# Kernel optimization log

Hardware: AMD Instinct MI355X
Metric: run time of the kernel (lower is better)

Reference implementation:

```python
import math
import jax, jax.numpy as jnp
import numpy as np

N_LAYERS = 2
D_MODEL = 512
D_STATE = 16
D_CONV = 4
D_INNER = 2 * D_MODEL          # expand = 2
DT_RANK = math.ceil(D_MODEL / 16)
BATCH = 16
SEQ = 2048
NUM_CLASSES = 1


def setup_inputs() -> dict:
    key = jax.random.key(0)
    ks = jax.random.split(key, 9)
    def rn(k, shape, scale=0.02):
        return jax.random.normal(k, shape, dtype=jnp.float32) * scale
    src       = jax.random.normal(ks[0], (BATCH, SEQ, D_MODEL), dtype=jnp.float32)
    norm_w    = jnp.ones((N_LAYERS, D_MODEL), jnp.float32)
    in_proj_W = rn(ks[1], (N_LAYERS, 2 * D_INNER, D_MODEL))
    conv_W    = rn(ks[2], (N_LAYERS, D_INNER, D_CONV), 0.1)
    conv_b    = jnp.zeros((N_LAYERS, D_INNER), jnp.float32)
    x_proj_W  = rn(ks[3], (N_LAYERS, DT_RANK + 2 * D_STATE, D_INNER))
    dt_proj_W = rn(ks[4], (N_LAYERS, D_INNER, DT_RANK), DT_RANK ** -0.5)
    dt_proj_b = rn(ks[5], (N_LAYERS, D_INNER), 0.1)
    # S4D-real init: A_n = n for n = 1..d_state, stored as log
    A_log     = jnp.log(jnp.broadcast_to(
        jnp.arange(1, D_STATE + 1, dtype=jnp.float32), (N_LAYERS, D_INNER, D_STATE)))
    D_skip    = jnp.ones((N_LAYERS, D_INNER), jnp.float32)
    out_proj_W = rn(ks[6], (N_LAYERS, D_MODEL, D_INNER))
    cls_W     = rn(ks[7], (NUM_CLASSES, D_MODEL))
    cls_b     = jnp.zeros((NUM_CLASSES,), jnp.float32)
    return dict(src=src, norm_w=norm_w, in_proj_W=in_proj_W, conv_W=conv_W,
                conv_b=conv_b, x_proj_W=x_proj_W, dt_proj_W=dt_proj_W,
                dt_proj_b=dt_proj_b, A_log=A_log, D_skip=D_skip,
                out_proj_W=out_proj_W, cls_W=cls_W, cls_b=cls_b)


def _rmsnorm(x, w, eps=1e-5):
    return x * jax.lax.rsqrt(jnp.mean(x * x, axis=-1, keepdims=True) + eps) * w


def _mamba_block(x, p):
    B, L, _ = x.shape
    xz = jnp.einsum('bld,ed->ble', x, p['in_proj_W'])      # (B,L,2*ED)
    xb, z = jnp.split(xz, 2, axis=-1)
    # causal depthwise conv along time
    xc = jax.lax.conv_general_dilated(
        xb.transpose(0, 2, 1), p['conv_W'][:, None, :], (1,),
        [(D_CONV - 1, 0)], feature_group_count=D_INNER,
        dimension_numbers=('NCH', 'OIH', 'NCH'))
    xc = (xc + p['conv_b'][None, :, None]).transpose(0, 2, 1)  # (B,L,ED)
    xc = jax.nn.silu(xc)
    # input-dependent SSM params
    dbc = jnp.einsum('ble,re->blr', xc, p['x_proj_W'])
    dt, Bm, Cm = jnp.split(dbc, [DT_RANK, DT_RANK + D_STATE], axis=-1)
    delta = jax.nn.softplus(
        jnp.einsum('blr,er->ble', dt, p['dt_proj_W']) + p['dt_proj_b'])
    A = -jnp.exp(p['A_log'])                                # (ED,N)

    def step(h, inp):
        d_t, B_t, C_t, x_t = inp                            # (B,ED),(B,N),(B,N),(B,ED)
        dA = jnp.exp(d_t[:, :, None] * A)                   # (B,ED,N)
        h = dA * h + d_t[:, :, None] * B_t[:, None, :] * x_t[:, :, None]
        y = jnp.einsum('ben,bn->be', h, C_t)
        return h, y

    h0 = jnp.zeros((B, D_INNER, D_STATE), xc.dtype)
    xs = (delta.transpose(1, 0, 2), Bm.transpose(1, 0, 2),
          Cm.transpose(1, 0, 2), xc.transpose(1, 0, 2))
    _, ys = jax.lax.scan(step, h0, xs)                      # (L,B,ED)
    y = ys.transpose(1, 0, 2) + p['D_skip'] * xc
    y = y * jax.nn.silu(z)
    return jnp.einsum('ble,de->bld', y, p['out_proj_W'])


def reference(src, norm_w, in_proj_W, conv_W, conv_b, x_proj_W, dt_proj_W,
              dt_proj_b, A_log, D_skip, out_proj_W, cls_W, cls_b):
    x = src
    for l in range(N_LAYERS):
        p = dict(in_proj_W=in_proj_W[l], conv_W=conv_W[l], conv_b=conv_b[l],
                 x_proj_W=x_proj_W[l], dt_proj_W=dt_proj_W[l],
                 dt_proj_b=dt_proj_b[l], A_log=A_log[l], D_skip=D_skip[l],
                 out_proj_W=out_proj_W[l])
        x = x + _mamba_block(_rmsnorm(x, norm_w[l]), p)
    pooled = x.mean(axis=1)                                  # (B, d_model)
    logits = pooled @ cls_W.T + cls_b
    return jax.nn.sigmoid(logits)
```

## Files before the change

### kernel.cpp

```cpp
#include <hip/hip_runtime.h>
#include <math.h>

#define DEV __device__ __forceinline__

constexpr int B_ = 16, L_ = 2048, DM = 512, DI = 1024, DS = 16;
constexpr int G_ = 64, CS = L_ / G_;

using f32x4  = __attribute__((ext_vector_type(4))) float;
using f2     = __attribute__((ext_vector_type(2))) float;
using bf16x8 = __attribute__((ext_vector_type(8))) __bf16;

DEV float bf2f(unsigned int u) { return __uint_as_float(u << 16); }
DEV unsigned short f2bf(float f) {
  unsigned u = __float_as_uint(f);
  u += 0x7fff + ((u >> 16) & 1);
  return (unsigned short)(u >> 16);
}
DEV float sigm(float x) { return 1.f / (1.f + __expf(-x)); }

constexpr size_t O_NORM  = 0;
constexpr size_t O_INPJ  = 1024;
constexpr size_t O_CONVW = 2098176;
constexpr size_t O_CONVB = 2106368;
constexpr size_t O_XPJ   = 2108416;
constexpr size_t O_DTW   = 2239488;
constexpr size_t O_DTB   = 2305024;
constexpr size_t O_ALOG  = 2307072;
constexpr size_t O_DSK   = 2339840;
constexpr size_t O_OUTW  = 2341888;
constexpr size_t O_CLSW  = 3390464;
constexpr size_t O_CLSB  = 3390976;
constexpr size_t CW_TOT  = 3390977;

DEV unsigned short cvt1(const void* p, size_t i, int bf) {
  return bf ? ((const unsigned short*)p)[i] : f2bf(((const float*)p)[i]);
}

__global__ void k_cvtw(const void* normw, const void* inpj, const void* convw, const void* convb,
                       const void* xpj,   const void* dtw,  const void* dtb,   const void* alog,
                       const void* dsk,   const void* outw, const void* clsw,  const void* clsb,
                       int* __restrict__ flag, float* __restrict__ logits,
                       unsigned short* __restrict__ dst) {
  const unsigned short* nw = (const unsigned short*)normw;
  int bf = 1;
  #pragma unroll
  for (int i = 0; i < 8; i += 2) bf &= (nw[i] == 0x3F80);
  size_t i = (size_t)blockIdx.x * 256 + threadIdx.x;
  if (i == 0) *flag = bf;
  if (i < 16 * 256) logits[i] = 0.f;
  if (i >= CW_TOT) return;
  unsigned short v;
  if      (i < O_INPJ)  v = cvt1(normw, i - O_NORM,  bf);
  else if (i < O_CONVW) v = cvt1(inpj,  i - O_INPJ,  bf);
  else if (i < O_CONVB) v = cvt1(convw, i - O_CONVW, bf);
  else if (i < O_XPJ)   v = cvt1(convb, i - O_CONVB, bf);
  else if (i < O_DTW)   v = cvt1(xpj,   i - O_XPJ,   bf);
  else if (i < O_DTB)   v = cvt1(dtw,   i - O_DTW,   bf);
  else if (i < O_ALOG)  v = cvt1(dtb,   i - O_DTB,   bf);
  else if (i < O_DSK)   v = cvt1(alog,  i - O_ALOG,  bf);
  else if (i < O_OUTW)  v = cvt1(dsk,   i - O_DSK,   bf);
  else if (i < O_CLSW)  v = cvt1(outw,  i - O_OUTW,  bf);
  else if (i < O_CLSB)  v = cvt1(clsw,  i - O_CLSW,  bf);
  else                  v = cvt1(clsb,  i - O_CLSB,  bf);
  dst[i] = v;
}

__global__ void k_rmsnorm0(const unsigned short* __restrict__ s16, const float* __restrict__ s32,
                           const int* __restrict__ flag, const unsigned short* __restrict__ w,
                           unsigned short* __restrict__ out, float* __restrict__ x) {
  int t = blockIdx.x, tid = threadIdx.x;
  int d = tid * 2;
  float2 v;
  if (*flag) {
    ushort2 u = ((const ushort2*)(s16 + (size_t)t * DM))[tid];
    v.x = bf2f(u.x); v.y = bf2f(u.y);
  } else {
    v = ((const float2*)(s32 + (size_t)t * DM))[tid];
  }
  ((float2*)(x + (size_t)t * DM))[tid] = v;
  float ss = v.x * v.x + v.y * v.y;
  #pragma unroll
  for (int m = 32; m; m >>= 1) ss += __shfl_xor(ss, m, 64);
  __shared__ float sr[4];
  if ((tid & 63) == 0) sr[tid >> 6] = ss;
  __syncthreads();
  float scale = rsqrtf((sr[0] + sr[1] + sr[2] + sr[3]) * (1.f / DM) + 1e-5f);
  unsigned short o0 = f2bf(v.x * scale * bf2f(w[d]));
  unsigned short o1 = f2bf(v.y * scale * bf2f(w[d + 1]));
  *(ushort2*)(out + (size_t)t * DM + d) = make_ushort2(o0, o1);
}

__global__ void k_rmsnorm1(const float* __restrict__ x, const unsigned short* __restrict__ w,
                           const unsigned short* __restrict__ clsW, float* __restrict__ lg,
                           unsigned short* __restrict__ out) {
  int t = blockIdx.x, tid = threadIdx.x;
  float2 v = ((const float2*)(x + (size_t)t * DM))[tid];
  int d = tid * 2;
  float ss = v.x * v.x + v.y * v.y;
  float cd = v.x * bf2f(clsW[d]) + v.y * bf2f(clsW[d + 1]);
  #pragma unroll
  for (int m = 32; m; m >>= 1) {
    ss += __shfl_xor(ss, m, 64);
    cd += __shfl_xor(cd, m, 64);
  }
  __shared__ float sr[4], sc[4];
  if ((tid & 63) == 0) { sr[tid >> 6] = ss; sc[tid >> 6] = cd; }
  __syncthreads();
  float scale = rsqrtf((sr[0] + sr[1] + sr[2] + sr[3]) * (1.f / DM) + 1e-5f);
  if (tid == 0)
    atomicAdd(&lg[(t >> 11) * 256 + (t & 255)], sc[0] + sc[1] + sc[2] + sc[3]);
  unsigned short o0 = f2bf(v.x * scale * bf2f(w[d]));
  unsigned short o1 = f2bf(v.y * scale * bf2f(w[d + 1]));
  *(ushort2*)(out + (size_t)t * DM + d) = make_ushort2(o0, o1);
}

DEV void async16(const void* g, void* l) {
  __builtin_amdgcn_global_load_lds((const __attribute__((address_space(1))) unsigned int*)g,
                                   (__attribute__((address_space(3))) unsigned int*)l, 16, 0, 0);
}

template <int BM, int BN, int EPI>
__global__ __launch_bounds__(256)
void k_gemm(const unsigned short* __restrict__ A, const unsigned short* __restrict__ B,
            void* __restrict__ C, int K, int lda, int ldb, int ldc,
            const unsigned short* __restrict__ bias, float* __restrict__ lg) {
  constexpr int BK = 32;
  constexpr int TM = BM / 32;
  constexpr int TN = BN / 32;
  __shared__ __align__(16) unsigned short sA[BM * BK];
  __shared__ __align__(16) unsigned short sB[BN * BK];
  const int tid = threadIdx.x;
  const int lane = tid & 63, wid = tid >> 6;
  const int wm = wid >> 1, wn = wid & 1;
  const int fr = lane & 15, fq = lane >> 4;

  int m0, n0;
  {
    const int nb = gridDim.x, mb = gridDim.y;
    if ((mb & 7) == 0) {
      int id = blockIdx.y * nb + blockIdx.x;
      int xcd = id & 7, slot = id >> 3;
      int mi = (xcd * (mb >> 3)) + slot / nb;
      int ni = slot % nb;
      m0 = mi * BM; n0 = ni * BN;
    } else {
      m0 = blockIdx.y * BM; n0 = blockIdx.x * BN;
    }
  }

  f32x4 acc[TM][TN];
  #pragma unroll
  for (int i = 0; i < TM; ++i)
    #pragma unroll
    for (int j = 0; j < TN; ++j) acc[i][j] = f32x4{0.f, 0.f, 0.f, 0.f};

  for (int kt = 0; kt < K; kt += BK) {
    #pragma unroll
    for (int i = 0; i < BM / 64; ++i) {
      int c = i * 256 + tid;
      async16(A + (size_t)(m0 + (c >> 2)) * lda + kt + (c & 3) * 8,
              &sA[(size_t)(i * 256 + (tid & 192)) * 8]);
    }
    #pragma unroll
    for (int i = 0; i < BN / 64; ++i) {
      int c = i * 256 + tid;
      async16(B + (size_t)(n0 + (c >> 2)) * ldb + kt + (c & 3) * 8,
              &sB[(size_t)(i * 256 + (tid & 192)) * 8]);
    }
    __syncthreads();
    bf16x8 af[TM], bg[TN];
    #pragma unroll
    for (int i = 0; i < TM; ++i)
      af[i] = *(const bf16x8*)&sA[(wm * (BM / 2) + i * 16 + fr) * BK + fq * 8];
    #pragma unroll
    for (int j = 0; j < TN; ++j)
      bg[j] = *(const bf16x8*)&sB[(wn * (BN / 2) + j * 16 + fr) * BK + fq * 8];
    #pragma unroll
    for (int i = 0; i < TM; ++i)
      #pragma unroll
      for (int j = 0; j < TN; ++j)
        acc[i][j] = __builtin_amdgcn_mfma_f32_16x16x32_bf16(af[i], bg[j], acc[i][j], 0, 0, 0);
    __syncthreads();
  }

  float cacc = 0.f;
  #pragma unroll
  for (int i = 0; i < TM; ++i) {
    int row = m0 + wm * (BM / 2) + i * 16 + fq * 4;
    #pragma unroll
    for (int j = 0; j < TN; ++j) {
      int col = n0 + wn * (BN / 2) + j * 16 + fr;
      #pragma unroll
      for (int r = 0; r < 4; ++r) {
        float v = acc[i][j][r];
        size_t off = (size_t)(row + r) * ldc + col;
        if constexpr (EPI == 0) {
          ((unsigned short*)C)[off] = f2bf(v);
        } else if constexpr (EPI == 1) {
          v += bf2f(bias[col]);
          v = (v > 20.f) ? v : __logf(1.f + __expf(v));
          ((unsigned short*)C)[off] = f2bf(v);
        } else if constexpr (EPI == 2) {
          ((float*)C)[off] += v;
        } else {
          cacc += v * bf2f(bias[col]);
        }
      }
    }
  }
  if constexpr (EPI == 4) {
    #pragma unroll
    for (int m = 32; m; m >>= 1) cacc += __shfl_xor(cacc, m, 64);
    __shared__ float sred[4];
    if (lane == 0) sred[wid] = cacc;
    __syncthreads();
    if (tid == 0)
      atomicAdd(&lg[(m0 >> 11) * 256 + ((m0 >> 6) & 255)],
                sred[0] + sred[1] + sred[2] + sred[3]);
  }
}

__global__ void k_conv(const unsigned short* __restrict__ xz, const unsigned short* __restrict__ W,
                       const unsigned short* __restrict__ bias, unsigned short* __restrict__ xc) {
  int idx = blockIdx.x * 256 + threadIdx.x;
  int eg = idx & 127;
  int t  = idx >> 7;
  int l  = t & (L_ - 1);
  int e0 = eg * 8;

  bf16x8 w0 = *(const bf16x8*)&W[e0 * 4];
  bf16x8 w1 = *(const bf16x8*)&W[e0 * 4 + 8];
  bf16x8 w2 = *(const bf16x8*)&W[e0 * 4 + 16];
  bf16x8 w3 = *(const bf16x8*)&W[e0 * 4 + 24];
  bf16x8 bs = *(const bf16x8*)&bias[e0];

  float acc[8];
  #pragma unroll
  for (int i = 0; i < 8; ++i) acc[i] = (float)bs[i];

  #pragma unroll
  for (int j = 0; j < 4; ++j) {
    if (l - 3 + j >= 0) {
      bf16x8 xr = *(const bf16x8*)&xz[((size_t)t + j - 3) * 2048 + e0];
      #pragma unroll
      for (int i = 0; i < 8; ++i) {
        const int wi = i * 4 + j;
        float wv = (wi < 8)  ? (float)w0[wi]      :
                   (wi < 16) ? (float)w1[wi - 8]  :
                   (wi < 24) ? (float)w2[wi - 16] : (float)w3[wi - 24];
        acc[i] += wv * (float)xr[i];
      }
    }
  }

  uint4 pk;
  unsigned o[8];
  #pragma unroll
  for (int i = 0; i < 8; ++i) {
    float v = acc[i];
    o[i] = f2bf(v * sigm(v));
  }
  pk.x = o[0] | (o[1] << 16);
  pk.y = o[2] | (o[3] << 16);
  pk.z = o[4] | (o[5] << 16);
  pk.w = o[6] | (o[7] << 16);
  *(uint4*)&xc[(size_t)t * DI + e0] = pk;
}

__global__ __launch_bounds__(256)
void k_scanA(const unsigned short* __restrict__ delta, const unsigned short* __restrict__ dbc,
             const unsigned short* __restrict__ xc,
             float* __restrict__ sumdl, unsigned short* __restrict__ xz) {
  const int tid = threadIdx.x;
  const int b  = blockIdx.x / (G_ * 4);
  const int r  = blockIdx.x % (G_ * 4);
  const int g  = r >> 2, eb = r & 3;
  const int e  = eb * 256 + tid;
  const size_t t0 = (size_t)b * L_ + (size_t)g * CS;

  __shared__ __align__(16) float sB[CS * 16];
  {
    int row = tid >> 3, c2 = tid & 7;
    ushort2 u = *(const ushort2*)&dbc[(t0 + row) * 64 + 32 + c2 * 2];
    sB[row * 16 + c2 * 2]     = bf2f(u.x);
    sB[row * 16 + c2 * 2 + 1] = bf2f(u.y);
  }
  __syncthreads();

  f2 h2[8];
  #pragma unroll
  for (int k = 0; k < 8; ++k) h2[k] = f2{0.f, 0.f};
  float sd = 0.f;

  const unsigned short* dp = delta + t0 * DI + e;
  const unsigned short* xp = xc + t0 * DI + e;
  for (int s = 0; s < CS; ++s) {
    float dl = bf2f(dp[(size_t)s * DI]);
    float xv = bf2f(xp[(size_t)s * DI]);
    sd += dl;
    float q = __expf(-dl);
    float q2 = q * q;
    f2 d = f2{q, q2};
    f2 qq = f2{q2, q2};
    f2 dlx = f2{dl * xv, dl * xv};
    const f2* Bp = (const f2*)&sB[s * 16];
    #pragma unroll
    for (int k = 0; k < 8; ++k) {
      h2[k] = d * h2[k] + Bp[k] * dlx;
      d *= qq;
    }
  }
  sumdl[((size_t)b * G_ + g) * DI + e] = sd;
  float* hz = (float*)xz + (t0 + (tid >> 3)) * 1024 + eb * 128 + (tid & 7) * 16;
  #pragma unroll
  for (int k = 0; k < 8; ++k) ((f2*)hz)[k] = h2[k];
}

__global__ void k_scanB(const float* __restrict__ sumdl, unsigned short* __restrict__ xz) {
  int id = blockIdx.x * 256 + threadIdx.x;
  int n = id & 15, e = (id >> 4) & (DI - 1), b = id >> 14;
  float An = -(float)(n + 1);
  float h = 0.f;
  size_t colOff = (size_t)((e >> 8) * 128 + (e & 7) * 16 + n);
  size_t rowBase = (size_t)b * L_ + ((e & 255) >> 3);
  for (int g = 0; g < G_; ++g) {
    float* hz = (float*)xz + (rowBase + (size_t)g * CS) * 1024 + colOff;
    float pA = __expf(An * sumdl[((size_t)b * G_ + g) * DI + e]);
    float ha = *hz;
    *hz = h;
    h = pA * h + ha;
  }
}

__global__ __launch_bounds__(256)
void k_scanC(unsigned short* __restrict__ dly, const unsigned short* __restrict__ dbc,
             const unsigned short* __restrict__ xc, const unsigned short* __restrict__ xz,
             const unsigned short* __restrict__ Dskip) {
  const int tid = threadIdx.x;
  const int b  = blockIdx.x / (G_ * 4);
  const int r  = blockIdx.x % (G_ * 4);
  const int g  = r >> 2, eb = r & 3;
  const int e  = eb * 256 + tid;
  const size_t t0 = (size_t)b * L_ + (size_t)g * CS;

  __shared__ __align__(16) float sBC[CS * 32];
  {
    int row = tid >> 3, quad = tid & 7;
    ushort4 u = *(const ushort4*)&dbc[(t0 + row) * 64 + 32 + quad * 4];
    float4 f;
    f.x = bf2f(u.x); f.y = bf2f(u.y); f.z = bf2f(u.z); f.w = bf2f(u.w);
    *(float4*)&sBC[row * 32 + quad * 4] = f;
  }
  __syncthreads();

  f2 h2[8];
  {
    const float* hz = (const float*)xz + (t0 + (tid >> 3)) * 1024 + eb * 128 + (tid & 7) * 16;
    #pragma unroll
    for (int k = 0; k < 8; ++k) h2[k] = ((const f2*)hz)[k];
  }

  float D = bf2f(Dskip[e]);
  unsigned short*       dp = dly + t0 * DI + e;
  const unsigned short* xp = xc + t0 * DI + e;
  const unsigned short* zp = xz + t0 * 2048 + 1024 + e;
  for (int s = 0; s < CS; ++s) {
    float dl = bf2f(dp[(size_t)s * DI]);
    float xv = bf2f(xp[(size_t)s * DI]);
    float q = __expf(-dl);
    float q2 = q * q;
    f2 d = f2{q, q2};
    f2 qq = f2{q2, q2};
    f2 dlx = f2{dl * xv, dl * xv};
    const f2* Bp = (const f2*)&sBC[s * 32];
    const f2* Cp = (const f2*)&sBC[s * 32 + 16];
    f2 p2 = f2{0.f, 0.f};
    #pragma unroll
    for (int k = 0; k < 8; ++k) {
      h2[k] = d * h2[k] + Bp[k] * dlx;
      p2 += h2[k] * Cp[k];
      d *= qq;
    }
    float p = p2.x + p2.y;
    float z = bf2f(zp[(size_t)s * 2048]);
    dp[(size_t)s * DI] = f2bf((p + D * xv) * (z * sigm(z)));
  }
}

__global__ void k_final(const float* __restrict__ lg, const unsigned short* __restrict__ clsb,
                        const int* __restrict__ flag, void* __restrict__ out) {
  int b = blockIdx.x, tid = threadIdx.x;
  float v = lg[b * 256 + tid];
  #pragma unroll
  for (int m = 32; m; m >>= 1) v += __shfl_xor(v, m, 64);
  __shared__ float sr[4];
  if ((tid & 63) == 0) sr[tid >> 6] = v;
  __syncthreads();
  if (tid == 0) {
    float s = sigm((sr[0] + sr[1] + sr[2] + sr[3]) * (1.f / L_) + bf2f(clsb[0]));
    if (*flag) ((unsigned short*)out)[b] = f2bf(s);
    else       ((float*)out)[b] = s;
  }
}

extern "C" void kernel_launch(void* const* d_in, const int* in_sizes, int n_in,
                              void* d_out, int out_size, void* d_ws, size_t ws_size,
                              hipStream_t stream) {
  char* base = (char*)d_ws;
  unsigned short* cw = (unsigned short*)base;
  int*   flag   = (int*)(base + 6782976);
  float* logits = (float*)(base + 6783040);
  const size_t fixed = 6783040 + 16 * 256 * 4;

  const size_t perBatch = (size_t)L_ * DM * 4 + (size_t)L_ * 2048 * 2 +
                          (size_t)L_ * DI * 2 + (size_t)L_ * DI * 2 +
                          (size_t)L_ * 64 * 2 + (size_t)G_ * DI * 4;
  int BCH = 16;
  while (BCH > 1 && fixed + perBatch * BCH > ws_size) BCH >>= 1;
  const size_t T = (size_t)BCH * L_;

  char* w = base + fixed;
  float* x              = (float*)w;          w += T * DM * 4;
  unsigned short* xz    = (unsigned short*)w; w += T * 2048 * 2;
  unsigned short* xc    = (unsigned short*)w; w += T * DI * 2;
  unsigned short* dxn   = (unsigned short*)w; w += T * DI * 2;
  unsigned short* dbc   = (unsigned short*)w; w += T * 64 * 2;
  float* sumdl          = (float*)w;

  k_cvtw<<<(int)((CW_TOT + 255) / 256), 256, 0, stream>>>(
      d_in[1], d_in[2], d_in[3], d_in[4], d_in[5], d_in[6], d_in[7], d_in[8],
      d_in[9], d_in[10], d_in[11], d_in[12], flag, logits, cw);

  for (int b0 = 0; b0 < B_; b0 += BCH) {
    const unsigned short* s16 = (const unsigned short*)d_in[0] + (size_t)b0 * L_ * DM;
    const float*          s32 = (const float*)d_in[0] + (size_t)b0 * L_ * DM;

    for (int l = 0; l < 2; ++l) {
      if (l == 0)
        k_rmsnorm0<<<(int)T, 256, 0, stream>>>(s16, s32, flag, cw + O_NORM, dxn, x);
      else
        k_rmsnorm1<<<(int)T, 256, 0, stream>>>(x, cw + O_NORM + DM, cw + O_CLSW,
                                               logits + (size_t)b0 * 256, dxn);
      k_gemm<128, 128, 0><<<dim3(16, (int)(T / 128)), 256, 0, stream>>>(
          dxn, cw + O_INPJ + (size_t)l * 2048 * 512, xz, 512, 512, 512, 2048,
          nullptr, nullptr);
      k_conv<<<(int)(T * 128 / 256), 256, 0, stream>>>(
          xz, cw + O_CONVW + l * DI * 4, cw + O_CONVB + l * DI, xc);
      k_gemm<64, 64, 0><<<dim3(1, (int)(T / 64)), 256, 0, stream>>>(
          xc, cw + O_XPJ + (size_t)l * 64 * DI, dbc, 1024, 1024, 1024, 64,
          nullptr, nullptr);
      k_gemm<128, 64, 1><<<dim3(16, (int)(T / 128)), 256, 0, stream>>>(
          dbc, cw + O_DTW + (size_t)l * DI * 32, dxn, 32, 64, 32, 1024,
          cw + O_DTB + l * DI, nullptr);
      k_scanA<<<BCH * G_ * 4, 256, 0, stream>>>(dxn, dbc, xc, sumdl, xz);
      k_scanB<<<BCH * 64, 256, 0, stream>>>(sumdl, xz);
      k_scanC<<<BCH * G_ * 4, 256, 0, stream>>>(dxn, dbc, xc, xz, cw + O_DSK + l * DI);
      if (l == 0)
        k_gemm<64, 64, 2><<<dim3(8, (int)(T / 64)), 256, 0, stream>>>(
            dxn, cw + O_OUTW, x, 1024, 1024, 1024, 512, nullptr, nullptr);
      else
        k_gemm<64, 64, 4><<<dim3(8, (int)(T / 64)), 256, 0, stream>>>(
            dxn, cw + O_OUTW + (size_t)DM * DI, nullptr, 1024, 1024, 1024, 512,
            cw + O_CLSW, logits + (size_t)b0 * 256);
    }
  }

  k_final<<<B_, 256, 0, stream>>>(logits, cw + O_CLSB, flag, d_out);
}
```

Baseline: 1.126 ms.

## Fuse dt projection into scans and fold final out_proj with classifier weights

Removes the separate dt_proj GEMM and computes delta per chunk inside scanA and scanC via small MFMA tiles with softplus into shared memory. This avoids writing and re-reading the delta tensor. The last layer's out_proj GEMM is dropped: out_proj is precomputed times cls_W into a vector w2, and scanC accumulates y·w2 straight into the logits. Layer 0's residual add now reads src inside the out_proj epilogue instead of rmsnorm0 storing x. In exchange, delta is recomputed in two kernels, shared memory per block grows (lower occupancy risk), and the folded math changes rounding order.

Result: faster. 1.026 ms (-8.9%).

```diff
diff --git a/kernel.cpp b/kernel.cpp
--- a/kernel.cpp
+++ b/kernel.cpp
@@ -17,6 +17,7 @@
   return (unsigned short)(u >> 16);
 }
 DEV float sigm(float x) { return 1.f / (1.f + __expf(-x)); }
+DEV float softp(float v) { return (v > 20.f) ? v : __logf(1.f + __expf(v)); }
 
 constexpr size_t O_NORM  = 0;
 constexpr size_t O_INPJ  = 1024;
@@ -65,9 +66,23 @@
   dst[i] = v;
 }
 
+__global__ void k_w2(const unsigned short* __restrict__ outw, const unsigned short* __restrict__ clsw,
+                     float* __restrict__ w2) {
+  int el = threadIdx.x & 63, dq = threadIdx.x >> 6;
+  int e = blockIdx.x * 64 + el;
+  float s = 0.f;
+  #pragma unroll 4
+  for (int d = dq * 128; d < dq * 128 + 128; ++d)
+    s += bf2f(outw[(size_t)d * DI + e]) * bf2f(clsw[d]);
+  __shared__ float sp[256];
+  sp[threadIdx.x] = s;
+  __syncthreads();
+  if (dq == 0) w2[e] = sp[el] + sp[64 + el] + sp[128 + el] + sp[192 + el];
+}
+
 __global__ void k_rmsnorm0(const unsigned short* __restrict__ s16, const float* __restrict__ s32,
                            const int* __restrict__ flag, const unsigned short* __restrict__ w,
-                           unsigned short* __restrict__ out, float* __restrict__ x) {
+                           unsigned short* __restrict__ out) {
   int t = blockIdx.x, tid = threadIdx.x;
   int d = tid * 2;
   float2 v;
@@ -77,7 +92,6 @@
   } else {
     v = ((const float2*)(s32 + (size_t)t * DM))[tid];
   }
-  ((float2*)(x + (size_t)t * DM))[tid] = v;
   float ss = v.x * v.x + v.y * v.y;
   #pragma unroll
   for (int m = 32; m; m >>= 1) ss += __shfl_xor(ss, m, 64);
@@ -123,7 +137,8 @@
 __global__ __launch_bounds__(256)
 void k_gemm(const unsigned short* __restrict__ A, const unsigned short* __restrict__ B,
             void* __restrict__ C, int K, int lda, int ldb, int ldc,
-            const unsigned short* __restrict__ bias, float* __restrict__ lg) {
+            const unsigned short* __restrict__ s16, const float* __restrict__ s32,
+            const int* __restrict__ flag) {
   constexpr int BK = 32;
   constexpr int TM = BM / 32;
   constexpr int TN = BN / 32;
@@ -183,7 +198,6 @@
     __syncthreads();
   }
 
-  float cacc = 0.f;
   #pragma unroll
   for (int i = 0; i < TM; ++i) {
     int row = m0 + wm * (BM / 2) + i * 16 + fq * 4;
@@ -196,27 +210,12 @@
         size_t off = (size_t)(row + r) * ldc + col;
         if constexpr (EPI == 0) {
           ((unsigned short*)C)[off] = f2bf(v);
-        } else if constexpr (EPI == 1) {
-          v += bf2f(bias[col]);
-          v = (v > 20.f) ? v : __logf(1.f + __expf(v));
-          ((unsigned short*)C)[off] = f2bf(v);
-        } else if constexpr (EPI == 2) {
-          ((float*)C)[off] += v;
         } else {
-          cacc += v * bf2f(bias[col]);
+          float sv = (*flag) ? bf2f(s16[off]) : s32[off];
+          ((float*)C)[off] = sv + v;
         }
       }
     }
-  }
-  if constexpr (EPI == 4) {
-    #pragma unroll
-    for (int m = 32; m; m >>= 1) cacc += __shfl_xor(cacc, m, 64);
-    __shared__ float sred[4];
-    if (lane == 0) sred[wid] = cacc;
-    __syncthreads();
-    if (tid == 0)
-      atomicAdd(&lg[(m0 >> 11) * 256 + ((m0 >> 6) & 255)],
-                sred[0] + sred[1] + sred[2] + sred[3]);
   }
 }
 
@@ -267,9 +266,32 @@
   *(uint4*)&xc[(size_t)t * DI + e0] = pk;
 }
 
+DEV void delta_tile(const unsigned short* __restrict__ dbc, size_t t0,
+                    const unsigned short* __restrict__ dtW,
+                    const unsigned short* __restrict__ dtb,
+                    int eb, int tid, float* __restrict__ sD) {
+  const int lane = tid & 63, wid = tid >> 6;
+  const int fr = lane & 15, fq = lane >> 4;
+  bf16x8 a0 = *(const bf16x8*)&dbc[(t0 + fr) * 64 + fq * 8];
+  bf16x8 a1 = *(const bf16x8*)&dbc[(t0 + 16 + fr) * 64 + fq * 8];
+  #pragma unroll
+  for (int j = 0; j < 4; ++j) {
+    const int ec = wid * 64 + j * 16 + fr;
+    bf16x8 bw = *(const bf16x8*)&dtW[(size_t)(eb * 256 + ec) * 32 + fq * 8];
+    f32x4 d0 = __builtin_amdgcn_mfma_f32_16x16x32_bf16(a0, bw, f32x4{0.f, 0.f, 0.f, 0.f}, 0, 0, 0);
+    f32x4 d1 = __builtin_amdgcn_mfma_f32_16x16x32_bf16(a1, bw, f32x4{0.f, 0.f, 0.f, 0.f}, 0, 0, 0);
+    float bi = bf2f(dtb[eb * 256 + ec]);
+    #pragma unroll
+    for (int r = 0; r < 4; ++r) {
+      sD[(fq * 4 + r) * 256 + ec]      = softp(d0[r] + bi);
+      sD[(16 + fq * 4 + r) * 256 + ec] = softp(d1[r] + bi);
+    }
+  }
+}
+
 __global__ __launch_bounds__(256)
-void k_scanA(const unsigned short* __restrict__ delta, const unsigned short* __restrict__ dbc,
-             const unsigned short* __restrict__ xc,
+void k_scanA(const unsigned short* __restrict__ dbc, const unsigned short* __restrict__ xc,
+             const unsigned short* __restrict__ dtW, const unsigned short* __restrict__ dtb,
              float* __restrict__ sumdl, unsigned short* __restrict__ xz) {
   const int tid = threadIdx.x;
   const int b  = blockIdx.x / (G_ * 4);
@@ -279,12 +301,14 @@
   const size_t t0 = (size_t)b * L_ + (size_t)g * CS;
 
   __shared__ __align__(16) float sB[CS * 16];
+  __shared__ __align__(16) float sD[CS * 256];
   {
     int row = tid >> 3, c2 = tid & 7;
     ushort2 u = *(const ushort2*)&dbc[(t0 + row) * 64 + 32 + c2 * 2];
     sB[row * 16 + c2 * 2]     = bf2f(u.x);
     sB[row * 16 + c2 * 2 + 1] = bf2f(u.y);
   }
+  delta_tile(dbc, t0, dtW, dtb, eb, tid, sD);
   __syncthreads();
 
   f2 h2[8];
@@ -292,10 +316,9 @@
   for (int k = 0; k < 8; ++k) h2[k] = f2{0.f, 0.f};
   float sd = 0.f;
 
-  const unsigned short* dp = delta + t0 * DI + e;
   const unsigned short* xp = xc + t0 * DI + e;
   for (int s = 0; s < CS; ++s) {
-    float dl = bf2f(dp[(size_t)s * DI]);
+    float dl = sD[s * 256 + tid];
     float xv = bf2f(xp[(size_t)s * DI]);
     sd += dl;
     float q = __expf(-dl);
@@ -332,10 +355,13 @@
   }
 }
 
+template <int LAST>
 __global__ __launch_bounds__(256)
-void k_scanC(unsigned short* __restrict__ dly, const unsigned short* __restrict__ dbc,
+void k_scanC(unsigned short* __restrict__ yout, const unsigned short* __restrict__ dbc,
              const unsigned short* __restrict__ xc, const unsigned short* __restrict__ xz,
-             const unsigned short* __restrict__ Dskip) {
+             const unsigned short* __restrict__ Dskip,
+             const unsigned short* __restrict__ dtW, const unsigned short* __restrict__ dtb,
+             const float* __restrict__ w2, float* __restrict__ lg) {
   const int tid = threadIdx.x;
   const int b  = blockIdx.x / (G_ * 4);
   const int r  = blockIdx.x % (G_ * 4);
@@ -344,6 +370,7 @@
   const size_t t0 = (size_t)b * L_ + (size_t)g * CS;
 
   __shared__ __align__(16) float sBC[CS * 32];
+  __shared__ __align__(16) float sD[CS * 256];
   {
     int row = tid >> 3, quad = tid & 7;
     ushort4 u = *(const ushort4*)&dbc[(t0 + row) * 64 + 32 + quad * 4];
@@ -351,6 +378,7 @@
     f.x = bf2f(u.x); f.y = bf2f(u.y); f.z = bf2f(u.z); f.w = bf2f(u.w);
     *(float4*)&sBC[row * 32 + quad * 4] = f;
   }
+  delta_tile(dbc, t0, dtW, dtb, eb, tid, sD);
   __syncthreads();
 
   f2 h2[8];
@@ -361,11 +389,13 @@
   }
 
   float D = bf2f(Dskip[e]);
-  unsigned short*       dp = dly + t0 * DI + e;
+  float wv = 0.f, la = 0.f;
+  if constexpr (LAST) wv = w2[e];
+  unsigned short*       yp = yout + t0 * DI + e;
   const unsigned short* xp = xc + t0 * DI + e;
   const unsigned short* zp = xz + t0 * 2048 + 1024 + e;
   for (int s = 0; s < CS; ++s) {
-    float dl = bf2f(dp[(size_t)s * DI]);
+    float dl = sD[s * 256 + tid];
     float xv = bf2f(xp[(size_t)s * DI]);
     float q = __expf(-dl);
     float q2 = q * q;
@@ -383,7 +413,18 @@
     }
     float p = p2.x + p2.y;
     float z = bf2f(zp[(size_t)s * 2048]);
-    dp[(size_t)s * DI] = f2bf((p + D * xv) * (z * sigm(z)));
+    float y = (p + D * xv) * (z * sigm(z));
+    if constexpr (LAST) la += y * wv;
+    else                yp[(size_t)s * DI] = f2bf(y);
+  }
+  if constexpr (LAST) {
+    #pragma unroll
+    for (int m = 32; m; m >>= 1) la += __shfl_xor(la, m, 64);
+    __shared__ float sr[4];
+    if ((tid & 63) == 0) sr[tid >> 6] = la;
+    __syncthreads();
+    if (tid == 0)
+      atomicAdd(&lg[b * 256 + (g * 4 + eb)], sr[0] + sr[1] + sr[2] + sr[3]);
   }
 }
 
@@ -410,7 +451,8 @@
   unsigned short* cw = (unsigned short*)base;
   int*   flag   = (int*)(base + 6782976);
   float* logits = (float*)(base + 6783040);
-  const size_t fixed = 6783040 + 16 * 256 * 4;
+  float* w2     = (float*)(base + 6799424);
+  const size_t fixed = 6799424 + 4096;
 
   const size_t perBatch = (size_t)L_ * DM * 4 + (size_t)L_ * 2048 * 2 +
                           (size_t)L_ * DI * 2 + (size_t)L_ * DI * 2 +
@@ -430,6 +472,7 @@
   k_cvtw<<<(int)((CW_TOT + 255) / 256), 256, 0, stream>>>(
       d_in[1], d_in[2], d_in[3], d_in[4], d_in[5], d_in[6], d_in[7], d_in[8],
       d_in[9], d_in[10], d_in[11], d_in[12], flag, logits, cw);
+  k_w2<<<16, 256, 0, stream>>>(cw + O_OUTW + (size_t)DM * DI, cw + O_CLSW, w2);
 
   for (int b0 = 0; b0 < B_; b0 += BCH) {
     const unsigned short* s16 = (const unsigned short*)d_in[0] + (size_t)b0 * L_ * DM;
@@ -437,31 +480,31 @@
 
     for (int l = 0; l < 2; ++l) {
       if (l == 0)
-        k_rmsnorm0<<<(int)T, 256, 0, stream>>>(s16, s32, flag, cw + O_NORM, dxn, x);
+        k_rmsnorm0<<<(int)T, 256, 0, stream>>>(s16, s32, flag, cw + O_NORM, dxn);
       else
         k_rmsnorm1<<<(int)T, 256, 0, stream>>>(x, cw + O_NORM + DM, cw + O_CLSW,
                                                logits + (size_t)b0 * 256, dxn);
       k_gemm<128, 128, 0><<<dim3(16, (int)(T / 128)), 256, 0, stream>>>(
           dxn, cw + O_INPJ + (size_t)l * 2048 * 512, xz, 512, 512, 512, 2048,
-          nullptr, nullptr);
+          nullptr, nullptr, nullptr);
       k_conv<<<(int)(T * 128 / 256), 256, 0, stream>>>(
           xz, cw + O_CONVW + l * DI * 4, cw + O_CONVB + l * DI, xc);
       k_gemm<64, 64, 0><<<dim3(1, (int)(T / 64)), 256, 0, stream>>>(
           xc, cw + O_XPJ + (size_t)l * 64 * DI, dbc, 1024, 1024, 1024, 64,
-          nullptr, nullptr);
-      k_gemm<128, 64, 1><<<dim3(16, (int)(T / 128)), 256, 0, stream>>>(
-          dbc, cw + O_DTW + (size_t)l * DI * 32, dxn, 32, 64, 32, 1024,
-          cw + O_DTB + l * DI, nullptr);
-      k_scanA<<<BCH * G_ * 4, 256, 0, stream>>>(dxn, dbc, xc, sumdl, xz);
+          nullptr, nullptr, nullptr);
+      k_scanA<<<BCH * G_ * 4, 256, 0, stream>>>(
+          dbc, xc, cw + O_DTW + (size_t)l * DI * 32, cw + O_DTB + l * DI, sumdl, xz);
       k_scanB<<<BCH * 64, 256, 0, stream>>>(sumdl, xz);
-      k_scanC<<<BCH * G_ * 4, 256, 0, stream>>>(dxn, dbc, xc, xz, cw + O_DSK + l * DI);
-      if (l == 0)
-        k_gemm<64, 64, 2><<<dim3(8, (int)(T / 64)), 256, 0, stream>>>(
-            dxn, cw + O_OUTW, x, 1024, 1024, 1024, 512, nullptr, nullptr);
-      else
-        k_gemm<64, 64, 4><<<dim3(8, (int)(T / 64)), 256, 0, stream>>>(
-            dxn, cw + O_OUTW + (size_t)DM * DI, nullptr, 1024, 1024, 1024, 512,
-            cw + O_CLSW, logits + (size_t)b0 * 256);
+      if (l == 0) {
+        k_scanC<0><<<BCH * G_ * 4, 256, 0, stream>>>(
+            dxn, dbc, xc, xz, cw + O_DSK, cw + O_DTW, cw + O_DTB, nullptr, nullptr);
+        k_gemm<64, 64, 3><<<dim3(8, (int)(T / 64)), 256, 0, stream>>>(
+            dxn, cw + O_OUTW, x, 1024, 1024, 1024, 512, s16, s32, flag);
+      } else {
+        k_scanC<1><<<BCH * G_ * 4, 256, 0, stream>>>(
+            nullptr, dbc, xc, xz, cw + O_DSK + DI, cw + O_DTW + (size_t)DI * 32,
+            cw + O_DTB + DI, w2, logits + (size_t)b0 * 256);
+      }
     }
   }
 
```
